# Performance work log

Measured on AMD Instinct MI355X. Metric: run time of the kernel, lower is better.

## Reference

```python
import jax, jax.numpy as jnp
import numpy as np

B, E, WIN, DX, DZ, RAW = 2048, 32, 10, 14, 14, 22

def _leaky(x):
    return jnp.where(x >= 0, x, 0.01 * x)

def setup_inputs():
    key = jax.random.key(0)
    ks = jax.random.split(key, 20)
    def w(k, i, o):
        return jax.random.normal(k, (i, o), dtype=jnp.float32) / np.float32(np.sqrt(i))
    def b(k, o):
        return jax.random.normal(k, (o,), dtype=jnp.float32) * 0.01
    return {
        "raw_obs": jax.random.normal(ks[0], (B, WIN, 1, RAW), dtype=jnp.float32),
        "state_prev": jax.random.normal(ks[1], (B, E, WIN, DX), dtype=jnp.float32),
        "pm_w1": w(ks[2], WIN * DX, 256), "pm_b1": b(ks[3], 256),
        "pm_w3": w(ks[4], 256, 512), "pm_b3": b(ks[5], 512),
        "pm_wm2": w(ks[6], 512, DX), "pm_bm2": b(ks[7], DX),
        "sm_w2": w(ks[8], WIN * RAW, 256), "sm_b2": b(ks[9], 256),
        "sm_w3": w(ks[10], 256, 256), "sm_b3": b(ks[11], 256),
        "sm_w5": w(ks[12], 256, 64), "sm_b5": b(ks[13], 64),
        "sm_w6": w(ks[14], 64, DZ), "sm_b6": b(ks[15], DZ),
        "on_w1": w(ks[16], DZ, 32), "on_b1": b(ks[17], 32),
        "on_w2": w(ks[18], 32, DZ), "on_b2": b(ks[19], DZ),
    }

def reference(raw_obs, state_prev, pm_w1, pm_b1, pm_w3, pm_b3, pm_wm2, pm_bm2,
              sm_w2, sm_b2, sm_w3, sm_b3, sm_w5, sm_b5, sm_w6, sm_b6,
              on_w1, on_b1, on_w2, on_b2):
    bs, ens, win, dx = state_prev.shape
    dz = sm_w6.shape[1]
    # --- process model (LinearFlipout evaluated at mean weights) ---
    x = state_prev.reshape(bs * ens, win * dx)
    x = _leaky(x @ pm_w1 + pm_b1)
    x = _leaky(x @ pm_w3 + pm_b3)
    state_pred = (x @ pm_wm2 + pm_bm2).reshape(bs, ens, dx)   # [B,E,dx]
    state_m = state_pred.mean(axis=1)                          # [B,dx]
    A = state_pred - state_m[:, None, :]                       # [B,E,dx]
    # --- sensor model: torch repeat(E,1,1,1) tiles ensemble-major, the final
    # reshape reinterprets as batch-major; replicate that layout faithfully ---
    s = jnp.tile(raw_obs, (ens, 1, 1, 1)).reshape(bs * ens, win * raw_obs.shape[-1])
    s = _leaky(s @ sm_w2 + sm_b2)
    s = _leaky(s @ sm_w3 + sm_b3)
    s = _leaky(s @ sm_w5 + sm_b5)
    s = s @ sm_w6 + sm_b6
    ensemble_z = s.reshape(bs, ens, dz)                        # [B,E,dz]
    z = ensemble_z.mean(axis=1, keepdims=True)                 # [B,1,dz]
    # --- observation noise R = diag_embed(square(mlp(z)+c) + init) ---
    r = jax.nn.relu(z @ on_w1 + on_b1) @ on_w2 + on_b2
    r = jnp.square(r + 0.001) + 0.038729833
    R = r.reshape(bs, dz)[:, :, None] * jnp.eye(dz, dtype=r.dtype)  # [B,dz,dz]
    # --- EnKF correction ---
    S = jnp.einsum('bei,bej->bij', A, A)                       # AT @ A, [B,dx,dx]
    innovation = S / (ens - 1) + R
    K = (S / (ens - 1)) @ jnp.linalg.inv(innovation)           # [B,dx,dz]
    diff = ensemble_z - state_pred                             # (y - H_XT)^T, [B,E,dz]
    gain = jnp.einsum('bij,bej->bei', K, diff)                 # [B,E,dx]
    state_corrected = state_pred + gain
    return (state_corrected,
            state_corrected.mean(axis=1, keepdims=True),
            state_m[:, None, :],
            z,
            ensemble_z)
```

## Files before the change

### kernel.cpp

```cpp
#include <hip/hip_runtime.h>

typedef unsigned short u16;
typedef __attribute__((ext_vector_type(8))) short short8;
typedef __attribute__((ext_vector_type(4))) float floatx4;

#define MFMA_BF16 __builtin_amdgcn_mfma_f32_16x16x32_bf16

__device__ __forceinline__ u16 f2bf(float f) {
    union { float f; unsigned int i; } v; v.f = f;
    unsigned int u = v.i;
    u += 0x7fffu + ((u >> 16) & 1u);
    return (u16)(u >> 16);
}
__device__ __forceinline__ float leaky(float x) { return x >= 0.f ? x : 0.01f * x; }

#define H1S 264
#define RS 232
#define H3S 72
#define CS 136

#define O1 917504
#define O2 946176
#define O3 974848
#define O4 1003520

#define PW1   0
#define PW3   40960
#define PWM2  172032
#define PSW2  180224
#define PSW3  237568
#define PSW5  303104
#define PSW6  319488
#define PTOTAL 320512
#define WS_NEEDED 641024
#define WS_BIG (641024 + 3670016)

struct PackSeg { const float* W; int K, N, S, base, count; };
struct PackArgs { PackSeg seg[7]; };

__global__ __launch_bounds__(256) void pack_all(PackArgs pa, u16* __restrict__ P) {
    int u = blockIdx.x * 256 + threadIdx.x;
    if (u >= PTOTAL) return;
#pragma unroll
    for (int i = 0; i < 7; i++) {
        if (u >= pa.seg[i].base && u < pa.seg[i].base + pa.seg[i].count) {
            int v = u - pa.seg[i].base;
            int j = v & 7;
            int l = (v >> 3) & 63;
            int ts = v >> 9;
            int s = ts % pa.seg[i].S;
            int t = ts / pa.seg[i].S;
            int k = s * 32 + (l >> 4) * 8 + j;
            int n = t * 16 + (l & 15);
            P[u] = (k < pa.seg[i].K && n < pa.seg[i].N)
                       ? f2bf(pa.seg[i].W[k * pa.seg[i].N + n]) : (u16)0;
            return;
        }
    }
}

__device__ __forceinline__ short8 load_x_frag(const float* __restrict__ X,
                                              int row, int s, int q) {
    const float* p = X + row * 140;
    float4 v0 = {0.f, 0.f, 0.f, 0.f}, v1 = {0.f, 0.f, 0.f, 0.f};
    int col0 = s * 32 + q * 8;
    if (s < 4) {
        v0 = *(const float4*)(p + col0);
        v1 = *(const float4*)(p + col0 + 4);
    } else {
        if (q <= 1) v0 = *(const float4*)(p + col0);
        if (q == 0) v1 = *(const float4*)(p + col0 + 4);
    }
    short8 r;
    r[0] = (short)f2bf(v0.x); r[1] = (short)f2bf(v0.y);
    r[2] = (short)f2bf(v0.z); r[3] = (short)f2bf(v0.w);
    r[4] = (short)f2bf(v1.x); r[5] = (short)f2bf(v1.y);
    r[6] = (short)f2bf(v1.z); r[7] = (short)f2bf(v1.w);
    return r;
}

__global__ __launch_bounds__(256, 5) void merged_mlp(
    const float* __restrict__ Rg, const float* __restrict__ Xg,
    const u16* __restrict__ Pk,
    const float* __restrict__ b1, const float* __restrict__ b3,
    const float* __restrict__ bm2,
    const float* __restrict__ b2, const float* __restrict__ sb3,
    const float* __restrict__ b5, const float* __restrict__ b6,
    float* __restrict__ ez_out,
    float* __restrict__ sp_ws)
{
    __shared__ __align__(16) u16 ldsH[32 * H1S];
    __shared__ __align__(16) u16 ldsC[32 * CS];

    const int tid  = threadIdx.x;
    const int lane = tid & 63;
    const int wave = tid >> 6;
    const int q    = lane >> 4;
    const int n16  = lane & 15;

    if (blockIdx.x < 64) {
        const u16* w2p = Pk + PSW2;
        const u16* w3p = Pk + PSW3;
        const u16* w5p = Pk + PSW5;
        const u16* w6p = Pk + PSW6;
        const int row0 = blockIdx.x * 32;

        for (int idx = tid; idx < 32 * 56; idx += 256) {
            int r = idx / 56, c4 = idx - r * 56;
            float4 v = {0.f, 0.f, 0.f, 0.f};
            if (c4 < 55) v = *(const float4*)&Rg[(row0 + r) * 220 + c4 * 4];
            u16* dst = &ldsH[r * RS + c4 * 4];
            dst[0] = f2bf(v.x); dst[1] = f2bf(v.y); dst[2] = f2bf(v.z); dst[3] = f2bf(v.w);
        }
        __syncthreads();

        floatx4 acc1[2][4];
        {
            floatx4 zero = {0.f, 0.f, 0.f, 0.f};
            for (int rt = 0; rt < 2; rt++)
                for (int ct = 0; ct < 4; ct++) acc1[rt][ct] = zero;
#pragma unroll
            for (int s = 0; s < 7; s++) {
                short8 a0 = *(const short8*)&ldsH[n16 * RS + s * 32 + q * 8];
                short8 a1 = *(const short8*)&ldsH[(n16 + 16) * RS + s * 32 + q * 8];
#pragma unroll
                for (int ct = 0; ct < 4; ct++) {
                    int t = wave * 4 + ct;
                    short8 bf = *(const short8*)&w2p[((t * 7 + s) * 64 + lane) * 8];
                    acc1[0][ct] = MFMA_BF16(a0, bf, acc1[0][ct], 0, 0, 0);
                    acc1[1][ct] = MFMA_BF16(a1, bf, acc1[1][ct], 0, 0, 0);
                }
            }
        }
        __syncthreads();
#pragma unroll
        for (int ct = 0; ct < 4; ct++) {
            int col = (wave * 4 + ct) * 16 + n16;
            float bias = b2[col];
#pragma unroll
            for (int rt = 0; rt < 2; rt++)
#pragma unroll
                for (int r = 0; r < 4; r++)
                    ldsH[(rt * 16 + q * 4 + r) * H1S + col] = f2bf(leaky(acc1[rt][ct][r] + bias));
        }
        __syncthreads();

        floatx4 acc5[2];
        {
            floatx4 zero = {0.f, 0.f, 0.f, 0.f};
            acc5[0] = zero; acc5[1] = zero;
        }
#pragma unroll
        for (int c = 0; c < 2; c++) {
            floatx4 zero = {0.f, 0.f, 0.f, 0.f};
            floatx4 acc[2][2];
            for (int rt = 0; rt < 2; rt++)
                for (int ct = 0; ct < 2; ct++) acc[rt][ct] = zero;
#pragma unroll
            for (int s = 0; s < 8; s++) {
                short8 a0 = *(const short8*)&ldsH[n16 * H1S + s * 32 + q * 8];
                short8 a1 = *(const short8*)&ldsH[(n16 + 16) * H1S + s * 32 + q * 8];
#pragma unroll
                for (int ct = 0; ct < 2; ct++) {
                    int tg = c * 8 + wave * 2 + ct;
                    short8 bf = *(const short8*)&w3p[((tg * 8 + s) * 64 + lane) * 8];
                    acc[0][ct] = MFMA_BF16(a0, bf, acc[0][ct], 0, 0, 0);
                    acc[1][ct] = MFMA_BF16(a1, bf, acc[1][ct], 0, 0, 0);
                }
            }
#pragma unroll
            for (int ct = 0; ct < 2; ct++) {
                int cl = (wave * 2 + ct) * 16 + n16;
                float bias = sb3[c * 128 + cl];
#pragma unroll
                for (int rt = 0; rt < 2; rt++)
#pragma unroll
                    for (int r = 0; r < 4; r++)
                        ldsC[(rt * 16 + q * 4 + r) * CS + cl] = f2bf(leaky(acc[rt][ct][r] + bias));
            }
            __syncthreads();
#pragma unroll
            for (int sl = 0; sl < 4; sl++) {
                int sg = c * 4 + sl;
                short8 bf = *(const short8*)&w5p[((wave * 8 + sg) * 64 + lane) * 8];
#pragma unroll
                for (int rt = 0; rt < 2; rt++) {
                    short8 a = *(const short8*)&ldsC[(rt * 16 + n16) * CS + sl * 32 + q * 8];
                    acc5[rt] = MFMA_BF16(a, bf, acc5[rt], 0, 0, 0);
                }
            }
            __syncthreads();
        }

        {
            int col = wave * 16 + n16;
            float bias = b5[col];
#pragma unroll
            for (int rt = 0; rt < 2; rt++)
#pragma unroll
                for (int r = 0; r < 4; r++)
                    ldsC[(rt * 16 + q * 4 + r) * H3S + col] = f2bf(leaky(acc5[rt][r] + bias));
        }
        __syncthreads();

        if (wave < 2) {
            floatx4 zero = {0.f, 0.f, 0.f, 0.f};
            floatx4 acc[2] = {zero, zero};
            int s = wave;
            short8 a0 = *(const short8*)&ldsC[n16 * H3S + s * 32 + q * 8];
            short8 a1 = *(const short8*)&ldsC[(n16 + 16) * H3S + s * 32 + q * 8];
            short8 bf = *(const short8*)&w6p[(s * 64 + lane) * 8];
            acc[0] = MFMA_BF16(a0, bf, acc[0], 0, 0, 0);
            acc[1] = MFMA_BF16(a1, bf, acc[1], 0, 0, 0);
            float* pacc = (float*)ldsH;
#pragma unroll
            for (int rt = 0; rt < 2; rt++)
#pragma unroll
                for (int r = 0; r < 4; r++)
                    pacc[(wave * 32 + rt * 16 + q * 4 + r) * 16 + n16] = acc[rt][r];
        }
        __syncthreads();
        {
            const float* pacc = (const float*)ldsH;
            for (int idx = tid; idx < 512; idx += 256) {
                int r = idx >> 4, c = idx & 15;
                float v = pacc[idx] + pacc[512 + idx];
                if (c < 14) ez_out[(row0 + r) * 14 + c] = v + b6[c];
            }
        }
    } else {
        const u16* w1p  = Pk + PW1;
        const u16* w3p  = Pk + PW3;
        const u16* wm2p = Pk + PWM2;
        const int bb   = blockIdx.x - 64;
        const int row0 = bb * 32;

        {
            floatx4 zero = {0.f, 0.f, 0.f, 0.f};
            floatx4 acc[2][4];
            for (int rt = 0; rt < 2; rt++)
                for (int ct = 0; ct < 4; ct++) acc[rt][ct] = zero;
#pragma unroll
            for (int s = 0; s < 5; s++) {
                short8 a0 = load_x_frag(Xg, row0 + n16, s, q);
                short8 a1 = load_x_frag(Xg, row0 + 16 + n16, s, q);
#pragma unroll
                for (int ct = 0; ct < 4; ct++) {
                    int t = wave * 4 + ct;
                    short8 bf = *(const short8*)&w1p[((t * 5 + s) * 64 + lane) * 8];
                    acc[0][ct] = MFMA_BF16(a0, bf, acc[0][ct], 0, 0, 0);
                    acc[1][ct] = MFMA_BF16(a1, bf, acc[1][ct], 0, 0, 0);
                }
            }
#pragma unroll
            for (int ct = 0; ct < 4; ct++) {
                int col = (wave * 4 + ct) * 16 + n16;
                float bias = b1[col];
#pragma unroll
                for (int rt = 0; rt < 2; rt++)
#pragma unroll
                    for (int r = 0; r < 4; r++)
                        ldsH[(rt * 16 + q * 4 + r) * H1S + col] = f2bf(leaky(acc[rt][ct][r] + bias));
            }
        }
        __syncthreads();

        floatx4 acc3[2];
        {
            floatx4 zero = {0.f, 0.f, 0.f, 0.f};
            acc3[0] = zero; acc3[1] = zero;
        }
#pragma unroll
        for (int c = 0; c < 4; c++) {
            floatx4 zero = {0.f, 0.f, 0.f, 0.f};
            floatx4 acc[2][2];
            for (int rt = 0; rt < 2; rt++)
                for (int ct = 0; ct < 2; ct++) acc[rt][ct] = zero;
#pragma unroll
            for (int s = 0; s < 8; s++) {
                short8 a0 = *(const short8*)&ldsH[n16 * H1S + s * 32 + q * 8];
                short8 a1 = *(const short8*)&ldsH[(n16 + 16) * H1S + s * 32 + q * 8];
#pragma unroll
                for (int ct = 0; ct < 2; ct++) {
                    int tg = c * 8 + wave * 2 + ct;
                    short8 bf = *(const short8*)&w3p[((tg * 8 + s) * 64 + lane) * 8];
                    acc[0][ct] = MFMA_BF16(a0, bf, acc[0][ct], 0, 0, 0);
                    acc[1][ct] = MFMA_BF16(a1, bf, acc[1][ct], 0, 0, 0);
                }
            }
#pragma unroll
            for (int ct = 0; ct < 2; ct++) {
                int cl = (wave * 2 + ct) * 16 + n16;
                float bias = b3[c * 128 + cl];
#pragma unroll
                for (int rt = 0; rt < 2; rt++)
#pragma unroll
                    for (int r = 0; r < 4; r++)
                        ldsC[(rt * 16 + q * 4 + r) * CS + cl] = f2bf(leaky(acc[rt][ct][r] + bias));
            }
            __syncthreads();
            {
                int sg = c * 4 + wave;
                short8 bf = *(const short8*)&wm2p[(sg * 64 + lane) * 8];
#pragma unroll
                for (int rt = 0; rt < 2; rt++) {
                    short8 a = *(const short8*)&ldsC[(rt * 16 + n16) * CS + wave * 32 + q * 8];
                    acc3[rt] = MFMA_BF16(a, bf, acc3[rt], 0, 0, 0);
                }
            }
            __syncthreads();
        }

        {
            float* pacc = (float*)ldsH;
#pragma unroll
            for (int rt = 0; rt < 2; rt++)
#pragma unroll
                for (int r = 0; r < 4; r++)
                    pacc[(wave * 32 + rt * 16 + q * 4 + r) * 16 + n16] = acc3[rt][r];
        }
        __syncthreads();
        {
            const float* pacc = (const float*)ldsH;
            for (int idx = tid; idx < 512; idx += 256) {
                int r = idx >> 4, c = idx & 15;
                float v = pacc[idx] + pacc[512 + idx] + pacc[1024 + idx] + pacc[1536 + idx];
                if (c < 14) sp_ws[(row0 + r) * 14 + c] = v + bm2[c];
            }
        }
    }
}

__global__ __launch_bounds__(256) void enkf_tail(
    const float* __restrict__ sp_all,
    const float* __restrict__ on_w1, const float* __restrict__ on_b1,
    const float* __restrict__ on_w2, const float* __restrict__ on_b2,
    float* out)
{
    __shared__ float spv[32][14];
    __shared__ float ezv[32][14];
    __shared__ float smv[14], zzv[14], rrv[14];
    __shared__ float M[14][14];
    __shared__ float G[14][28];
    __shared__ float Kmat[14][14];
    __shared__ float fac[14];
    __shared__ float hbuf[32];

    const int tid = threadIdx.x;
    const int b = blockIdx.x;

    for (int idx = tid; idx < 448; idx += 256) ((float*)spv)[idx] = sp_all[b * 448 + idx];
    {
        const float* ezsrc = out + O4 + (b & 63) * 448;
        for (int idx = tid; idx < 448; idx += 256) ((float*)ezv)[idx] = ezsrc[idx];
    }
    __syncthreads();

    if (tid < 14) {
        float s = 0.f;
        for (int e = 0; e < 32; e++) s += spv[e][tid];
        smv[tid] = s * (1.f / 32.f);
    } else if (tid >= 32 && tid < 46) {
        int c = tid - 32;
        float s = 0.f;
        for (int e = 0; e < 32; e++) s += ezv[e][c];
        zzv[c] = s * (1.f / 32.f);
    }
    __syncthreads();

    if (tid < 196) {
        int i = tid / 14, j = tid - i * 14;
        float mi = smv[i], mj = smv[j];
        float s = 0.f;
        for (int e = 0; e < 32; e++) s += (spv[e][i] - mi) * (spv[e][j] - mj);
        M[i][j] = s * (1.f / 31.f);
    } else if (tid >= 224) {
        int l = tid - 224;
        float t = on_b1[l];
        for (int k = 0; k < 14; k++) t += zzv[k] * on_w1[k * 32 + l];
        hbuf[l] = t > 0.f ? t : 0.f;
    }
    __syncthreads();

    if (tid < 14) {
        float t = on_b2[tid];
        for (int k = 0; k < 32; k++) t += hbuf[k] * on_w2[k * 14 + tid];
        t += 0.001f;
        rrv[tid] = t * t + 0.038729833f;
    }
    __syncthreads();

    for (int idx = tid; idx < 392; idx += 256) {
        int i = idx / 28, j = idx - i * 28;
        G[i][j] = (j < 14) ? (M[i][j] + (i == j ? rrv[i] : 0.f))
                           : ((j - 14 == i) ? 1.f : 0.f);
    }
    __syncthreads();

    for (int c = 0; c < 14; c++) {
        if (tid < 64) {
            float pinv = 1.f / G[c][c];
            if (tid < 28) G[c][tid] *= pinv;
            if (tid < 14 && tid != c) fac[tid] = G[tid][c];
        }
        __syncthreads();
        for (int idx = tid; idx < 392; idx += 256) {
            int i = idx / 28, j = idx - i * 28;
            if (i != c) G[i][j] -= fac[i] * G[c][j];
        }
        __syncthreads();
    }

    if (tid < 196) {
        int i = tid / 14, j = tid - i * 14;
        float s = 0.f;
        for (int k = 0; k < 14; k++) s += M[i][k] * G[k][14 + j];
        Kmat[i][j] = s;
    }
    __syncthreads();

    for (int idx = tid; idx < 448; idx += 256) {
        int e = idx / 14, i = idx - e * 14;
        float g = 0.f;
        for (int j = 0; j < 14; j++) g += Kmat[i][j] * (ezv[e][j] - spv[e][j]);
        out[b * 448 + idx] = spv[e][i] + g;
        out[O4 + b * 448 + idx] = ezv[e][i];
    }
    if (tid < 14) {
        float g = 0.f;
        for (int j = 0; j < 14; j++) g += Kmat[tid][j] * (zzv[j] - smv[j]);
        out[O1 + b * 14 + tid] = smv[tid] + g;
        out[O2 + b * 14 + tid] = smv[tid];
        out[O3 + b * 14 + tid] = zzv[tid];
    }
}

extern "C" void kernel_launch(void* const* d_in, const int* in_sizes, int n_in,
                              void* d_out, int out_size, void* d_ws, size_t ws_size,
                              hipStream_t stream) {
    (void)in_sizes; (void)n_in; (void)out_size; (void)ws_size;

    const float* raw_obs    = (const float*)d_in[0];
    const float* state_prev = (const float*)d_in[1];
    const float* pm_w1  = (const float*)d_in[2];
    const float* pm_b1  = (const float*)d_in[3];
    const float* pm_w3  = (const float*)d_in[4];
    const float* pm_b3  = (const float*)d_in[5];
    const float* pm_wm2 = (const float*)d_in[6];
    const float* pm_bm2 = (const float*)d_in[7];
    const float* sm_w2  = (const float*)d_in[8];
    const float* sm_b2  = (const float*)d_in[9];
    const float* sm_w3  = (const float*)d_in[10];
    const float* sm_b3  = (const float*)d_in[11];
    const float* sm_w5  = (const float*)d_in[12];
    const float* sm_b5  = (const float*)d_in[13];
    const float* sm_w6  = (const float*)d_in[14];
    const float* sm_b6  = (const float*)d_in[15];
    const float* on_w1  = (const float*)d_in[16];
    const float* on_b1  = (const float*)d_in[17];
    const float* on_w2  = (const float*)d_in[18];
    const float* on_b2  = (const float*)d_in[19];

    float* out = (float*)d_out;
    u16* P = (u16*)d_ws;
    float* sp_ws = (float*)((char*)d_ws + WS_NEEDED);

    PackArgs pa;
    pa.seg[0] = { pm_w1,  140, 256, 5,  PW1,  40960  };
    pa.seg[1] = { pm_w3,  256, 512, 8,  PW3,  131072 };
    pa.seg[2] = { pm_wm2, 512, 14,  16, PWM2, 8192   };
    pa.seg[3] = { sm_w2,  220, 256, 7,  PSW2, 57344  };
    pa.seg[4] = { sm_w3,  256, 256, 8,  PSW3, 65536  };
    pa.seg[5] = { sm_w5,  256, 64,  8,  PSW5, 16384  };
    pa.seg[6] = { sm_w6,  64,  14,  2,  PSW6, 1024   };
    pack_all<<<(PTOTAL + 255) / 256, 256, 0, stream>>>(pa, P);

    merged_mlp<<<2112, 256, 0, stream>>>(raw_obs, state_prev, P,
                                         pm_b1, pm_b3, pm_bm2,
                                         sm_b2, sm_b3, sm_b5, sm_b6,
                                         out + O4, sp_ws);
    enkf_tail<<<2048, 256, 0, stream>>>(sp_ws, on_w1, on_b1, on_w2, on_b2, out);
}
```

Before: 174.0 us.

## Double MLP row tile to 64 with 512-thread blocks and stage X in LDS

The merged MLP kernel now processes 64 rows per block with 8 waves instead of 32 rows with 4 waves. Each weight fragment loaded from global memory is reused across 4 row tiles instead of 2, which halves weight traffic per row. The process-model input is staged into LDS as bf16 before the first layer instead of being converted directly from global memory. Later layers are re-partitioned across the 8 waves with split-K partial sums reduced through LDS. The trade-off is much larger LDS use per block (about 67 KB), which limits occupancy, plus more accumulator registers per thread.

New measurement: 166.8 us. -4.1%, faster.

```diff
diff --git a/kernel.cpp b/kernel.cpp
--- a/kernel.cpp
+++ b/kernel.cpp
@@ -16,8 +16,8 @@
 
 #define H1S 264
 #define RS 232
+#define XS 168
 #define H3S 72
-#define CS 136
 
 #define O1 917504
 #define O2 946176
@@ -59,27 +59,7 @@
     }
 }
 
-__device__ __forceinline__ short8 load_x_frag(const float* __restrict__ X,
-                                              int row, int s, int q) {
-    const float* p = X + row * 140;
-    float4 v0 = {0.f, 0.f, 0.f, 0.f}, v1 = {0.f, 0.f, 0.f, 0.f};
-    int col0 = s * 32 + q * 8;
-    if (s < 4) {
-        v0 = *(const float4*)(p + col0);
-        v1 = *(const float4*)(p + col0 + 4);
-    } else {
-        if (q <= 1) v0 = *(const float4*)(p + col0);
-        if (q == 0) v1 = *(const float4*)(p + col0 + 4);
-    }
-    short8 r;
-    r[0] = (short)f2bf(v0.x); r[1] = (short)f2bf(v0.y);
-    r[2] = (short)f2bf(v0.z); r[3] = (short)f2bf(v0.w);
-    r[4] = (short)f2bf(v1.x); r[5] = (short)f2bf(v1.y);
-    r[6] = (short)f2bf(v1.z); r[7] = (short)f2bf(v1.w);
-    return r;
-}
-
-__global__ __launch_bounds__(256, 5) void merged_mlp(
+__global__ __launch_bounds__(512, 4) void merged_mlp(
     const float* __restrict__ Rg, const float* __restrict__ Xg,
     const u16* __restrict__ Pk,
     const float* __restrict__ b1, const float* __restrict__ b3,
@@ -89,8 +69,8 @@
     float* __restrict__ ez_out,
     float* __restrict__ sp_ws)
 {
-    __shared__ __align__(16) u16 ldsH[32 * H1S];
-    __shared__ __align__(16) u16 ldsC[32 * CS];
+    __shared__ __align__(16) u16 ldsH[64 * H1S];
+    __shared__ __align__(16) u16 ldsC[64 * H1S];
 
     const int tid  = threadIdx.x;
     const int lane = tid & 63;
@@ -98,14 +78,14 @@
     const int q    = lane >> 4;
     const int n16  = lane & 15;
 
-    if (blockIdx.x < 64) {
+    if (blockIdx.x < 32) {
         const u16* w2p = Pk + PSW2;
         const u16* w3p = Pk + PSW3;
         const u16* w5p = Pk + PSW5;
         const u16* w6p = Pk + PSW6;
-        const int row0 = blockIdx.x * 32;
-
-        for (int idx = tid; idx < 32 * 56; idx += 256) {
+        const int row0 = blockIdx.x * 64;
+
+        for (int idx = tid; idx < 64 * 56; idx += 512) {
             int r = idx / 56, c4 = idx - r * 56;
             float4 v = {0.f, 0.f, 0.f, 0.f};
             if (c4 < 55) v = *(const float4*)&Rg[(row0 + r) * 220 + c4 * 4];
@@ -114,117 +94,138 @@
         }
         __syncthreads();
 
-        floatx4 acc1[2][4];
-        {
-            floatx4 zero = {0.f, 0.f, 0.f, 0.f};
-            for (int rt = 0; rt < 2; rt++)
-                for (int ct = 0; ct < 4; ct++) acc1[rt][ct] = zero;
+        floatx4 acc1[4][2];
+        {
+            floatx4 zero = {0.f, 0.f, 0.f, 0.f};
+#pragma unroll
+            for (int rt = 0; rt < 4; rt++)
+#pragma unroll
+                for (int ct = 0; ct < 2; ct++) acc1[rt][ct] = zero;
 #pragma unroll
             for (int s = 0; s < 7; s++) {
-                short8 a0 = *(const short8*)&ldsH[n16 * RS + s * 32 + q * 8];
-                short8 a1 = *(const short8*)&ldsH[(n16 + 16) * RS + s * 32 + q * 8];
-#pragma unroll
-                for (int ct = 0; ct < 4; ct++) {
-                    int t = wave * 4 + ct;
+                short8 a[4];
+#pragma unroll
+                for (int rt = 0; rt < 4; rt++)
+                    a[rt] = *(const short8*)&ldsH[(rt * 16 + n16) * RS + s * 32 + q * 8];
+#pragma unroll
+                for (int ct = 0; ct < 2; ct++) {
+                    int t = wave * 2 + ct;
                     short8 bf = *(const short8*)&w2p[((t * 7 + s) * 64 + lane) * 8];
-                    acc1[0][ct] = MFMA_BF16(a0, bf, acc1[0][ct], 0, 0, 0);
-                    acc1[1][ct] = MFMA_BF16(a1, bf, acc1[1][ct], 0, 0, 0);
+#pragma unroll
+                    for (int rt = 0; rt < 4; rt++)
+                        acc1[rt][ct] = MFMA_BF16(a[rt], bf, acc1[rt][ct], 0, 0, 0);
                 }
             }
         }
         __syncthreads();
 #pragma unroll
-        for (int ct = 0; ct < 4; ct++) {
-            int col = (wave * 4 + ct) * 16 + n16;
+        for (int ct = 0; ct < 2; ct++) {
+            int col = (wave * 2 + ct) * 16 + n16;
             float bias = b2[col];
 #pragma unroll
-            for (int rt = 0; rt < 2; rt++)
+            for (int rt = 0; rt < 4; rt++)
 #pragma unroll
                 for (int r = 0; r < 4; r++)
                     ldsH[(rt * 16 + q * 4 + r) * H1S + col] = f2bf(leaky(acc1[rt][ct][r] + bias));
         }
         __syncthreads();
 
-        floatx4 acc5[2];
-        {
-            floatx4 zero = {0.f, 0.f, 0.f, 0.f};
-            acc5[0] = zero; acc5[1] = zero;
-        }
-#pragma unroll
-        for (int c = 0; c < 2; c++) {
-            floatx4 zero = {0.f, 0.f, 0.f, 0.f};
-            floatx4 acc[2][2];
-            for (int rt = 0; rt < 2; rt++)
+        {
+            floatx4 zero = {0.f, 0.f, 0.f, 0.f};
+            floatx4 acc[4][2];
+#pragma unroll
+            for (int rt = 0; rt < 4; rt++)
+#pragma unroll
                 for (int ct = 0; ct < 2; ct++) acc[rt][ct] = zero;
 #pragma unroll
             for (int s = 0; s < 8; s++) {
-                short8 a0 = *(const short8*)&ldsH[n16 * H1S + s * 32 + q * 8];
-                short8 a1 = *(const short8*)&ldsH[(n16 + 16) * H1S + s * 32 + q * 8];
+                short8 a[4];
+#pragma unroll
+                for (int rt = 0; rt < 4; rt++)
+                    a[rt] = *(const short8*)&ldsH[(rt * 16 + n16) * H1S + s * 32 + q * 8];
 #pragma unroll
                 for (int ct = 0; ct < 2; ct++) {
-                    int tg = c * 8 + wave * 2 + ct;
-                    short8 bf = *(const short8*)&w3p[((tg * 8 + s) * 64 + lane) * 8];
-                    acc[0][ct] = MFMA_BF16(a0, bf, acc[0][ct], 0, 0, 0);
-                    acc[1][ct] = MFMA_BF16(a1, bf, acc[1][ct], 0, 0, 0);
+                    int t = wave * 2 + ct;
+                    short8 bf = *(const short8*)&w3p[((t * 8 + s) * 64 + lane) * 8];
+#pragma unroll
+                    for (int rt = 0; rt < 4; rt++)
+                        acc[rt][ct] = MFMA_BF16(a[rt], bf, acc[rt][ct], 0, 0, 0);
                 }
             }
 #pragma unroll
             for (int ct = 0; ct < 2; ct++) {
                 int cl = (wave * 2 + ct) * 16 + n16;
-                float bias = sb3[c * 128 + cl];
-#pragma unroll
-                for (int rt = 0; rt < 2; rt++)
+                float bias = sb3[cl];
+#pragma unroll
+                for (int rt = 0; rt < 4; rt++)
 #pragma unroll
                     for (int r = 0; r < 4; r++)
-                        ldsC[(rt * 16 + q * 4 + r) * CS + cl] = f2bf(leaky(acc[rt][ct][r] + bias));
-            }
-            __syncthreads();
-#pragma unroll
-            for (int sl = 0; sl < 4; sl++) {
-                int sg = c * 4 + sl;
-                short8 bf = *(const short8*)&w5p[((wave * 8 + sg) * 64 + lane) * 8];
-#pragma unroll
-                for (int rt = 0; rt < 2; rt++) {
-                    short8 a = *(const short8*)&ldsC[(rt * 16 + n16) * CS + sl * 32 + q * 8];
+                        ldsC[(rt * 16 + q * 4 + r) * H1S + cl] = f2bf(leaky(acc[rt][ct][r] + bias));
+            }
+        }
+        __syncthreads();
+
+        floatx4 acc5[4];
+        {
+            floatx4 zero = {0.f, 0.f, 0.f, 0.f};
+#pragma unroll
+            for (int rt = 0; rt < 4; rt++) acc5[rt] = zero;
+            int t5 = wave >> 1, sh = wave & 1;
+#pragma unroll
+            for (int u = 0; u < 4; u++) {
+                int s = sh * 4 + u;
+                short8 bf = *(const short8*)&w5p[((t5 * 8 + s) * 64 + lane) * 8];
+#pragma unroll
+                for (int rt = 0; rt < 4; rt++) {
+                    short8 a = *(const short8*)&ldsC[(rt * 16 + n16) * H1S + s * 32 + q * 8];
                     acc5[rt] = MFMA_BF16(a, bf, acc5[rt], 0, 0, 0);
                 }
             }
-            __syncthreads();
-        }
-
-        {
-            int col = wave * 16 + n16;
-            float bias = b5[col];
+        }
+        {
+            float* pacc = (float*)ldsH;
+            int p = wave & 1, t5 = wave >> 1;
+#pragma unroll
+            for (int rt = 0; rt < 4; rt++)
+#pragma unroll
+                for (int r = 0; r < 4; r++)
+                    pacc[(p * 64 + rt * 16 + q * 4 + r) * 64 + t5 * 16 + n16] = acc5[rt][r];
+        }
+        __syncthreads();
+
+        {
+            const float* pacc = (const float*)ldsH;
+            for (int idx = tid; idx < 4096; idx += 512) {
+                int row = idx >> 6, col = idx & 63;
+                float v = pacc[row * 64 + col] + pacc[(64 + row) * 64 + col];
+                ldsC[row * H3S + col] = f2bf(leaky(v + b5[col]));
+            }
+        }
+        __syncthreads();
+
+        if (wave < 4) {
+            floatx4 zero = {0.f, 0.f, 0.f, 0.f};
+            floatx4 acc[2] = {zero, zero};
+            int s = wave & 1, rh = wave >> 1;
+            short8 bf = *(const short8*)&w6p[(s * 64 + lane) * 8];
+#pragma unroll
+            for (int rt = 0; rt < 2; rt++) {
+                short8 a = *(const short8*)&ldsC[(rh * 32 + rt * 16 + n16) * H3S + s * 32 + q * 8];
+                acc[rt] = MFMA_BF16(a, bf, acc[rt], 0, 0, 0);
+            }
+            float* pacc2 = (float*)ldsH;
 #pragma unroll
             for (int rt = 0; rt < 2; rt++)
 #pragma unroll
                 for (int r = 0; r < 4; r++)
-                    ldsC[(rt * 16 + q * 4 + r) * H3S + col] = f2bf(leaky(acc5[rt][r] + bias));
-        }
-        __syncthreads();
-
-        if (wave < 2) {
-            floatx4 zero = {0.f, 0.f, 0.f, 0.f};
-            floatx4 acc[2] = {zero, zero};
-            int s = wave;
-            short8 a0 = *(const short8*)&ldsC[n16 * H3S + s * 32 + q * 8];
-            short8 a1 = *(const short8*)&ldsC[(n16 + 16) * H3S + s * 32 + q * 8];
-            short8 bf = *(const short8*)&w6p[(s * 64 + lane) * 8];
-            acc[0] = MFMA_BF16(a0, bf, acc[0], 0, 0, 0);
-            acc[1] = MFMA_BF16(a1, bf, acc[1], 0, 0, 0);
-            float* pacc = (float*)ldsH;
-#pragma unroll
-            for (int rt = 0; rt < 2; rt++)
-#pragma unroll
-                for (int r = 0; r < 4; r++)
-                    pacc[(wave * 32 + rt * 16 + q * 4 + r) * 16 + n16] = acc[rt][r];
-        }
-        __syncthreads();
-        {
-            const float* pacc = (const float*)ldsH;
-            for (int idx = tid; idx < 512; idx += 256) {
+                    pacc2[(s * 64 + rh * 32 + rt * 16 + q * 4 + r) * 16 + n16] = acc[rt][r];
+        }
+        __syncthreads();
+        {
+            const float* pacc2 = (const float*)ldsH;
+            for (int idx = tid; idx < 1024; idx += 512) {
                 int r = idx >> 4, c = idx & 15;
-                float v = pacc[idx] + pacc[512 + idx];
+                float v = pacc2[r * 16 + c] + pacc2[(64 + r) * 16 + c];
                 if (c < 14) ez_out[(row0 + r) * 14 + c] = v + b6[c];
             }
         }
@@ -232,36 +233,51 @@
         const u16* w1p  = Pk + PW1;
         const u16* w3p  = Pk + PW3;
         const u16* wm2p = Pk + PWM2;
-        const int bb   = blockIdx.x - 64;
-        const int row0 = bb * 32;
-
-        {
-            floatx4 zero = {0.f, 0.f, 0.f, 0.f};
-            floatx4 acc[2][4];
-            for (int rt = 0; rt < 2; rt++)
-                for (int ct = 0; ct < 4; ct++) acc[rt][ct] = zero;
+        const int bb   = blockIdx.x - 32;
+        const int row0 = bb * 64;
+
+        for (int idx = tid; idx < 64 * 42; idx += 512) {
+            int r = idx / 42, c4 = idx - r * 42;
+            float4 v = {0.f, 0.f, 0.f, 0.f};
+            if (c4 < 35) v = *(const float4*)&Xg[(row0 + r) * 140 + c4 * 4];
+            u16* dst = &ldsH[r * XS + c4 * 4];
+            dst[0] = f2bf(v.x); dst[1] = f2bf(v.y); dst[2] = f2bf(v.z); dst[3] = f2bf(v.w);
+        }
+        __syncthreads();
+
+        floatx4 acc1[4][2];
+        {
+            floatx4 zero = {0.f, 0.f, 0.f, 0.f};
+#pragma unroll
+            for (int rt = 0; rt < 4; rt++)
+#pragma unroll
+                for (int ct = 0; ct < 2; ct++) acc1[rt][ct] = zero;
 #pragma unroll
             for (int s = 0; s < 5; s++) {
-                short8 a0 = load_x_frag(Xg, row0 + n16, s, q);
-                short8 a1 = load_x_frag(Xg, row0 + 16 + n16, s, q);
-#pragma unroll
-                for (int ct = 0; ct < 4; ct++) {
-                    int t = wave * 4 + ct;
+                short8 a[4];
+#pragma unroll
+                for (int rt = 0; rt < 4; rt++)
+                    a[rt] = *(const short8*)&ldsH[(rt * 16 + n16) * XS + s * 32 + q * 8];
+#pragma unroll
+                for (int ct = 0; ct < 2; ct++) {
+                    int t = wave * 2 + ct;
                     short8 bf = *(const short8*)&w1p[((t * 5 + s) * 64 + lane) * 8];
-                    acc[0][ct] = MFMA_BF16(a0, bf, acc[0][ct], 0, 0, 0);
-                    acc[1][ct] = MFMA_BF16(a1, bf, acc[1][ct], 0, 0, 0);
+#pragma unroll
+                    for (int rt = 0; rt < 4; rt++)
+                        acc1[rt][ct] = MFMA_BF16(a[rt], bf, acc1[rt][ct], 0, 0, 0);
                 }
             }
-#pragma unroll
-            for (int ct = 0; ct < 4; ct++) {
-                int col = (wave * 4 + ct) * 16 + n16;
-                float bias = b1[col];
-#pragma unroll
-                for (int rt = 0; rt < 2; rt++)
-#pragma unroll
-                    for (int r = 0; r < 4; r++)
-                        ldsH[(rt * 16 + q * 4 + r) * H1S + col] = f2bf(leaky(acc[rt][ct][r] + bias));
-            }
+        }
+        __syncthreads();
+#pragma unroll
+        for (int ct = 0; ct < 2; ct++) {
+            int col = (wave * 2 + ct) * 16 + n16;
+            float bias = b1[col];
+#pragma unroll
+            for (int rt = 0; rt < 4; rt++)
+#pragma unroll
+                for (int r = 0; r < 4; r++)
+                    ldsH[(rt * 16 + q * 4 + r) * H1S + col] = f2bf(leaky(acc1[rt][ct][r] + bias));
         }
         __syncthreads();
 
@@ -270,41 +286,49 @@
             floatx4 zero = {0.f, 0.f, 0.f, 0.f};
             acc3[0] = zero; acc3[1] = zero;
         }
-#pragma unroll
-        for (int c = 0; c < 4; c++) {
-            floatx4 zero = {0.f, 0.f, 0.f, 0.f};
-            floatx4 acc[2][2];
-            for (int rt = 0; rt < 2; rt++)
+        const int h = wave >> 2;
+        const int pg = wave & 3;
+#pragma unroll
+        for (int c = 0; c < 2; c++) {
+            floatx4 zero = {0.f, 0.f, 0.f, 0.f};
+            floatx4 acc[4][2];
+#pragma unroll
+            for (int rt = 0; rt < 4; rt++)
+#pragma unroll
                 for (int ct = 0; ct < 2; ct++) acc[rt][ct] = zero;
 #pragma unroll
             for (int s = 0; s < 8; s++) {
-                short8 a0 = *(const short8*)&ldsH[n16 * H1S + s * 32 + q * 8];
-                short8 a1 = *(const short8*)&ldsH[(n16 + 16) * H1S + s * 32 + q * 8];
+                short8 a[4];
+#pragma unroll
+                for (int rt = 0; rt < 4; rt++)
+                    a[rt] = *(const short8*)&ldsH[(rt * 16 + n16) * H1S + s * 32 + q * 8];
 #pragma unroll
                 for (int ct = 0; ct < 2; ct++) {
-                    int tg = c * 8 + wave * 2 + ct;
+                    int tg = c * 16 + wave * 2 + ct;
                     short8 bf = *(const short8*)&w3p[((tg * 8 + s) * 64 + lane) * 8];
-                    acc[0][ct] = MFMA_BF16(a0, bf, acc[0][ct], 0, 0, 0);
-                    acc[1][ct] = MFMA_BF16(a1, bf, acc[1][ct], 0, 0, 0);
+#pragma unroll
+                    for (int rt = 0; rt < 4; rt++)
+                        acc[rt][ct] = MFMA_BF16(a[rt], bf, acc[rt][ct], 0, 0, 0);
                 }
             }
 #pragma unroll
             for (int ct = 0; ct < 2; ct++) {
                 int cl = (wave * 2 + ct) * 16 + n16;
-                float bias = b3[c * 128 + cl];
-#pragma unroll
-                for (int rt = 0; rt < 2; rt++)
+                float bias = b3[c * 256 + cl];
+#pragma unroll
+                for (int rt = 0; rt < 4; rt++)
 #pragma unroll
                     for (int r = 0; r < 4; r++)
-                        ldsC[(rt * 16 + q * 4 + r) * CS + cl] = f2bf(leaky(acc[rt][ct][r] + bias));
+                        ldsC[(rt * 16 + q * 4 + r) * H1S + cl] = f2bf(leaky(acc[rt][ct][r] + bias));
             }
             __syncthreads();
-            {
-                int sg = c * 4 + wave;
-                short8 bf = *(const short8*)&wm2p[(sg * 64 + lane) * 8];
+#pragma unroll
+            for (int u = 0; u < 2; u++) {
+                int sgl = pg * 2 + u;
+                short8 bf = *(const short8*)&wm2p[((c * 8 + sgl) * 64 + lane) * 8];
 #pragma unroll
                 for (int rt = 0; rt < 2; rt++) {
-                    short8 a = *(const short8*)&ldsC[(rt * 16 + n16) * CS + wave * 32 + q * 8];
+                    short8 a = *(const short8*)&ldsC[(h * 32 + rt * 16 + n16) * H1S + sgl * 32 + q * 8];
                     acc3[rt] = MFMA_BF16(a, bf, acc3[rt], 0, 0, 0);
                 }
             }
@@ -317,14 +341,15 @@
             for (int rt = 0; rt < 2; rt++)
 #pragma unroll
                 for (int r = 0; r < 4; r++)
-                    pacc[(wave * 32 + rt * 16 + q * 4 + r) * 16 + n16] = acc3[rt][r];
+                    pacc[(pg * 64 + h * 32 + rt * 16 + q * 4 + r) * 16 + n16] = acc3[rt][r];
         }
         __syncthreads();
         {
             const float* pacc = (const float*)ldsH;
-            for (int idx = tid; idx < 512; idx += 256) {
+            for (int idx = tid; idx < 1024; idx += 512) {
                 int r = idx >> 4, c = idx & 15;
-                float v = pacc[idx] + pacc[512 + idx] + pacc[1024 + idx] + pacc[1536 + idx];
+                float v = pacc[r * 16 + c] + pacc[(64 + r) * 16 + c]
+                        + pacc[(128 + r) * 16 + c] + pacc[(192 + r) * 16 + c];
                 if (c < 14) sp_ws[(row0 + r) * 14 + c] = v + bm2[c];
             }
         }
@@ -475,7 +500,7 @@
     pa.seg[6] = { sm_w6,  64,  14,  2,  PSW6, 1024   };
     pack_all<<<(PTOTAL + 255) / 256, 256, 0, stream>>>(pa, P);
 
-    merged_mlp<<<2112, 256, 0, stream>>>(raw_obs, state_prev, P,
+    merged_mlp<<<1056, 512, 0, stream>>>(raw_obs, state_prev, P,
                                          pm_b1, pm_b3, pm_bm2,
                                          sm_b2, sm_b3, sm_b5, sm_b6,
                                          out + O4, sp_ws);
```
